# Performance work log

Measured on AMD Instinct MI355X. Metric: run time of the kernel, lower is better.

## Reference

```python
import jax, jax.numpy as jnp
import numpy as np

N_NODES = 100000
N_EDGES = 1600000
D_IN = 128
D_OUT = 128


def setup_inputs() -> dict:
    key = jax.random.key(0)
    k1, k2, k3 = jax.random.split(key, 3)
    x = jax.random.normal(k1, (N_NODES, D_IN), dtype=jnp.float32)
    edge_index = jax.random.randint(k2, (2, N_EDGES), 0, N_NODES, dtype=jnp.int32)
    W = jax.random.normal(k3, (D_IN, D_OUT), dtype=jnp.float32) / np.sqrt(D_IN)
    b = jnp.zeros((D_OUT,), dtype=jnp.float32)
    return {"x": x, "edge_index": edge_index, "W": W, "b": b}


def reference(x, edge_index, W, b):
    """GCNConv (add self-loops, symmetric norm) + ReLU.
    out = relu(D^-1/2 (A+I) D^-1/2 X W + b)
    """
    N = x.shape[0]
    src, dst = edge_index[0], edge_index[1]
    loop = jnp.arange(N, dtype=src.dtype)
    src = jnp.concatenate([src, loop])  # [E+N]
    dst = jnp.concatenate([dst, loop])  # [E+N]

    # degree of target nodes (includes self-loop, so deg >= 1)
    deg = jax.ops.segment_sum(jnp.ones(dst.shape, dtype=x.dtype), dst,
                              num_segments=N)
    deg_inv_sqrt = jax.lax.rsqrt(deg)
    norm = deg_inv_sqrt[src] * deg_inv_sqrt[dst]  # [E+N]

    h = x @ W  # [N, D_OUT] — transform before aggregation (PyG GCNConv)
    msg = h[src] * norm[:, None]  # gather + normalize
    out = jax.ops.segment_sum(msg, dst, num_segments=N)  # scatter-add
    return jax.nn.relu(out + b)
```

## Files before the change

kernel.cpp:

```cpp
#include <hip/hip_runtime.h>

#define N_NODES 100000
#define N_EDGES 1600000
#define D 128
#define SUBW 64
#define NSUB 1563
#define NC 98
#define CAPC 20480
#define CAP3 18432
#define CAPS 2048
#define CHUNK3 4096
#define BIND_BLOCKS ((N_EDGES + CHUNK3 - 1) / CHUNK3)
#define STAGE_MAX (CHUNK3 + NC * 16)
#define CCSTRIDE 16

typedef __attribute__((ext_vector_type(8))) short short8;
typedef __attribute__((ext_vector_type(4))) float float4v;

__device__ inline unsigned short f2bf(float f) {
    unsigned u = __float_as_uint(f);
    unsigned r = (u + 0x7fffu + ((u >> 16) & 1u)) >> 16;
    return (unsigned short)r;
}
__device__ inline float bflo(unsigned int p) { return __uint_as_float(p << 16); }
__device__ inline float bfhi(unsigned int p) { return __uint_as_float(p & 0xffff0000u); }

__global__ void probe_convert_kernel(const unsigned int* __restrict__ xw,
                                     const void* __restrict__ b,
                                     int* __restrict__ flag, float* __restrict__ bfv) {
    __shared__ int cnt;
    if (threadIdx.x == 0) cnt = 0;
    __syncthreads();
    unsigned low = xw[threadIdx.x] & 0xFFFFu;
    unsigned e = (low >> 7) & 0xFFu;
    atomicAdd(&cnt, (int)((e == 0u) || (e >= 107u && e <= 147u)));
    __syncthreads();
    int m = (cnt >= 192);
    if (threadIdx.x == 0) *flag = m;
    if (threadIdx.x < D)
        bfv[threadIdx.x] = m ? bflo(((const unsigned short*)b)[threadIdx.x])
                             : ((const float*)b)[threadIdx.x];
}

__global__ void __launch_bounds__(256) binD_kernel(
        const int* __restrict__ src, const int* __restrict__ dst,
        int* __restrict__ ccnt, unsigned* __restrict__ recg) {
    __shared__ __align__(16) unsigned stg[STAGE_MAX];
    __shared__ int cnt[NC], cpad[NC], ofs[NC], base[NC], place[NC];
    __shared__ int tot;

    int tid = threadIdx.x;
    int e0 = blockIdx.x * CHUNK3;
    int e1 = e0 + CHUNK3 < N_EDGES ? e0 + CHUNK3 : N_EDGES;
    if (tid < NC) cnt[tid] = 0;
    __syncthreads();

    unsigned recs[16];
    int bks[16];
    #pragma unroll
    for (int k = 0; k < 4; ++k) {
        int i = e0 + tid * 4 + k * 1024;
        if (i + 3 < e1) {
            int4 d4 = *(const int4*)&dst[i];
            int4 s4 = *(const int4*)&src[i];
            recs[k * 4 + 0] = (unsigned)s4.x | ((unsigned)(d4.x & 1023) << 17); bks[k * 4 + 0] = d4.x >> 10;
            recs[k * 4 + 1] = (unsigned)s4.y | ((unsigned)(d4.y & 1023) << 17); bks[k * 4 + 1] = d4.y >> 10;
            recs[k * 4 + 2] = (unsigned)s4.z | ((unsigned)(d4.z & 1023) << 17); bks[k * 4 + 2] = d4.z >> 10;
            recs[k * 4 + 3] = (unsigned)s4.w | ((unsigned)(d4.w & 1023) << 17); bks[k * 4 + 3] = d4.w >> 10;
        } else {
            bks[k * 4 + 0] = -1; bks[k * 4 + 1] = -1; bks[k * 4 + 2] = -1; bks[k * 4 + 3] = -1;
            recs[k * 4 + 0] = 0; recs[k * 4 + 1] = 0; recs[k * 4 + 2] = 0; recs[k * 4 + 3] = 0;
        }
    }
    #pragma unroll
    for (int k = 0; k < 16; ++k)
        if (bks[k] >= 0) atomicAdd(&cnt[bks[k]], 1);
    __syncthreads();

    if (tid < NC) {
        int c = cnt[tid];
        int p = (c + 15) & ~15;
        cpad[tid] = p;
        base[tid] = p ? atomicAdd(&ccnt[tid * CCSTRIDE], p) : 0;
    }
    __syncthreads();
    if (tid == 0) {
        int s = 0;
        for (int k = 0; k < NC; ++k) { ofs[k] = s; place[k] = s; s += cpad[k]; }
        tot = s;
    }
    __syncthreads();
    if (tid < NC) {
        int e = ofs[tid] + cpad[tid];
        for (int j = ofs[tid] + cnt[tid]; j < e; ++j) stg[j] = 0xFFFFFFFFu;
    }
    __syncthreads();

    #pragma unroll
    for (int k = 0; k < 16; ++k)
        if (bks[k] >= 0) {
            int p = atomicAdd(&place[bks[k]], 1);
            stg[p] = recs[k];
        }
    __syncthreads();

    int tot_ = tot;
    for (int j = tid * 4; j < tot_; j += 1024) {
        int lo = 0, hi = NC - 1;
        while (lo < hi) { int mid = (lo + hi + 1) >> 1; if (ofs[mid] <= j) lo = mid; else hi = mid - 1; }
        int gi = base[lo] + (j - ofs[lo]);
        if (gi < CAPC)
            *(uint4*)&recg[(size_t)lo * CAPC + gi] = *(const uint4*)&stg[j];
    }
}

__global__ void __launch_bounds__(256) sortdeg_kernel(
        unsigned* __restrict__ recg, const int* __restrict__ ccnt,
        int* __restrict__ deg, int* __restrict__ nodeofs) {
    __shared__ int hist[1024];
    __shared__ int ofs[1024];
    __shared__ int place[1024];
    __shared__ int wsum[4];
    __shared__ __align__(16) unsigned s_srt[CAP3];

    int b = blockIdx.x, tid = threadIdx.x;
    for (int t = tid; t < 1024; t += 256) hist[t] = 0;
    __syncthreads();
    int count = ccnt[b * CCSTRIDE]; if (count > CAPC) count = CAPC;
    const unsigned* r = recg + (size_t)b * CAPC;
    for (int i = tid * 4; i + 3 < count; i += 1024) {
        uint4 w4 = *(const uint4*)&r[i];
        if (w4.x != 0xFFFFFFFFu) atomicAdd(&hist[w4.x >> 17], 1);
        if (w4.y != 0xFFFFFFFFu) atomicAdd(&hist[w4.y >> 17], 1);
        if (w4.z != 0xFFFFFFFFu) atomicAdd(&hist[w4.z >> 17], 1);
        if (w4.w != 0xFFFFFFFFu) atomicAdd(&hist[w4.w >> 17], 1);
    }
    __syncthreads();

    int h0 = hist[tid * 4], h1 = hist[tid * 4 + 1];
    int h2 = hist[tid * 4 + 2], h3 = hist[tid * 4 + 3];
    int tot_t = h0 + h1 + h2 + h3;
    int lane = tid & 63, wave = tid >> 6;
    int v = tot_t;
    #pragma unroll
    for (int dsh = 1; dsh < 64; dsh <<= 1) {
        int u = __shfl_up(v, dsh);
        if (lane >= dsh) v += u;
    }
    if (lane == 63) wsum[wave] = v;
    __syncthreads();
    int wbase = 0;
    #pragma unroll
    for (int k = 0; k < 4; ++k) if (k < wave) wbase += wsum[k];
    int e0v = wbase + v - tot_t;
    ofs[tid * 4]     = e0v;           place[tid * 4]     = e0v;
    ofs[tid * 4 + 1] = e0v + h0;      place[tid * 4 + 1] = e0v + h0;
    ofs[tid * 4 + 2] = e0v + h0 + h1; place[tid * 4 + 2] = e0v + h0 + h1;
    ofs[tid * 4 + 3] = e0v + h0 + h1 + h2;
    place[tid * 4 + 3] = e0v + h0 + h1 + h2;
    int n4 = b * 1024 + tid * 4;
    *(int4*)&deg[n4]     = make_int4(h0, h1, h2, h3);
    *(int4*)&nodeofs[n4] = make_int4(e0v, e0v + h0, e0v + h0 + h1, e0v + h0 + h1 + h2);
    __syncthreads();

    for (int i = tid * 4; i + 3 < count; i += 1024) {
        uint4 w4 = *(const uint4*)&r[i];
        if (w4.x != 0xFFFFFFFFu) { int p = atomicAdd(&place[w4.x >> 17], 1); if (p < CAP3) s_srt[p] = w4.x & 0x1FFFFu; }
        if (w4.y != 0xFFFFFFFFu) { int p = atomicAdd(&place[w4.y >> 17], 1); if (p < CAP3) s_srt[p] = w4.y & 0x1FFFFu; }
        if (w4.z != 0xFFFFFFFFu) { int p = atomicAdd(&place[w4.z >> 17], 1); if (p < CAP3) s_srt[p] = w4.z & 0x1FFFFu; }
        if (w4.w != 0xFFFFFFFFu) { int p = atomicAdd(&place[w4.w >> 17], 1); if (p < CAP3) s_srt[p] = w4.w & 0x1FFFFu; }
    }
    __syncthreads();

    int total = ofs[1023] + hist[1023];
    int totR = (total + 15) & ~15; if (totR > CAP3) totR = CAP3;
    unsigned* w = recg + (size_t)b * CAPC;
    for (int j = tid * 4; j < totR; j += 1024)
        *(uint4*)&w[j] = *(const uint4*)&s_srt[j];
}

__global__ void gemm_kernel(const void* __restrict__ xv, const void* __restrict__ Wv,
                            const int* __restrict__ flag, const int* __restrict__ deg,
                            unsigned short* __restrict__ h) {
    __shared__ unsigned short Wt[D * 136];
    int tid = threadIdx.x;
    int m = *flag;
    for (int idx = tid; idx < D * D; idx += 256) {
        int k = idx >> 7, c = idx & 127;
        Wt[c * 136 + k] = m ? ((const unsigned short*)Wv)[idx]
                            : f2bf(((const float*)Wv)[idx]);
    }
    __syncthreads();

    int wave = tid >> 6, lane = tid & 63;
    int row0 = (blockIdx.x * 4 + wave) * 16;
    if (row0 >= N_NODES) return;
    int r = lane & 15, quad = lane >> 4;

    short8 a[4];
    if (m) {
        const unsigned short* xr = (const unsigned short*)xv + (size_t)(row0 + r) * D + quad * 8;
        #pragma unroll
        for (int t = 0; t < 4; ++t) a[t] = *(const short8*)(xr + t * 32);
    } else {
        const float* xr = (const float*)xv + (size_t)(row0 + r) * D + quad * 8;
        #pragma unroll
        for (int t = 0; t < 4; ++t)
            for (int j = 0; j < 8; ++j) a[t][j] = (short)f2bf(xr[t * 32 + j]);
    }

    float sc[4];
    #pragma unroll
    for (int reg = 0; reg < 4; ++reg)
        sc[reg] = rsqrtf((float)(deg[row0 + quad * 4 + reg] + 1));

    #pragma unroll
    for (int ct = 0; ct < 8; ++ct) {
        int col0 = ct * 16;
        float4v c = {0.f, 0.f, 0.f, 0.f};
        #pragma unroll
        for (int t = 0; t < 4; ++t) {
            short8 bfr = *(const short8*)&Wt[(col0 + r) * 136 + t * 32 + quad * 8];
            c = __builtin_amdgcn_mfma_f32_16x16x32_bf16(a[t], bfr, c, 0, 0, 0);
        }
        #pragma unroll
        for (int reg = 0; reg < 4; ++reg) {
            int orow = row0 + quad * 4 + reg;
            h[(size_t)orow * D + col0 + r] = f2bf(c[reg] * sc[reg]);
        }
    }
}

__global__ void __launch_bounds__(256) agg4_kernel(
        const unsigned* __restrict__ srt2, const int* __restrict__ nodeofs,
        const int* __restrict__ deg,
        const float* __restrict__ bfv, const int* __restrict__ flag,
        const unsigned short* __restrict__ h, void* __restrict__ out) {
    __shared__ unsigned srt[CAPS];
    __shared__ int l_ofs[SUBW];
    __shared__ int l_deg[SUBW];
    __shared__ float lbias[D];

    int sub = blockIdx.x, tid = threadIdx.x;
    int n0 = sub * SUBW;
    int B = sub >> 4, loc0 = (sub & 15) * SUBW;
    if (tid < SUBW) {
        l_ofs[tid] = nodeofs[B * 1024 + loc0 + tid];
        int n = n0 + tid;
        l_deg[tid] = (n < N_NODES) ? deg[n] : 0;
    }
    if (tid < D) lbias[tid] = bfv[tid];
    __syncthreads();

    int base0 = l_ofs[0];
    int span = (l_ofs[SUBW - 1] + l_deg[SUBW - 1]) - base0;
    if (span > CAPS) span = CAPS;
    if (span > CAP3 - base0) span = CAP3 - base0;
    const unsigned* sb = srt2 + (size_t)B * CAPC + base0;
    for (int i = tid; i < span; i += 256) srt[i] = sb[i];
    __syncthreads();

    const uint4* h4 = (const uint4*)h;
    int wave = tid >> 6, lane = tid & 63;
    int q = lane >> 4, c16 = lane & 15;
    int m = *flag;

    for (int t = 0; t < 16; ++t) {
        int nl = wave * 16 + t;
        int n = n0 + nl;
        if (n >= N_NODES) break;
        int o = l_ofs[nl] - base0;
        int cnt = l_deg[nl];
        int e_end = o + cnt; if (e_end > span) e_end = span;

        uint4 sp = make_uint4(0u, 0u, 0u, 0u);
        if (q == 0) sp = h4[(size_t)n * 16 + c16];

        float acc[8] = {0.f, 0.f, 0.f, 0.f, 0.f, 0.f, 0.f, 0.f};
        int j = o + q;
        for (; j + 4 < e_end; j += 8) {
            unsigned s0 = srt[j];
            unsigned s1 = srt[j + 4];
            uint4 p0 = h4[(size_t)s0 * 16 + c16];
            uint4 p1 = h4[(size_t)s1 * 16 + c16];
            acc[0] += bflo(p0.x); acc[1] += bfhi(p0.x);
            acc[2] += bflo(p0.y); acc[3] += bfhi(p0.y);
            acc[4] += bflo(p0.z); acc[5] += bfhi(p0.z);
            acc[6] += bflo(p0.w); acc[7] += bfhi(p0.w);
            acc[0] += bflo(p1.x); acc[1] += bfhi(p1.x);
            acc[2] += bflo(p1.y); acc[3] += bfhi(p1.y);
            acc[4] += bflo(p1.z); acc[5] += bfhi(p1.z);
            acc[6] += bflo(p1.w); acc[7] += bfhi(p1.w);
        }
        if (j < e_end) {
            unsigned s0 = srt[j];
            uint4 p0 = h4[(size_t)s0 * 16 + c16];
            acc[0] += bflo(p0.x); acc[1] += bfhi(p0.x);
            acc[2] += bflo(p0.y); acc[3] += bfhi(p0.y);
            acc[4] += bflo(p0.z); acc[5] += bfhi(p0.z);
            acc[6] += bflo(p0.w); acc[7] += bfhi(p0.w);
        }
        #pragma unroll
        for (int i = 0; i < 8; ++i) {
            acc[i] += __shfl_xor(acc[i], 16);
            acc[i] += __shfl_xor(acc[i], 32);
        }

        if (q == 0) {
            float dn = rsqrtf((float)(cnt + 1));
            float v[8];
            v[0] = fmaxf(dn * (acc[0] + bflo(sp.x)) + lbias[c16 * 8 + 0], 0.f);
            v[1] = fmaxf(dn * (acc[1] + bfhi(sp.x)) + lbias[c16 * 8 + 1], 0.f);
            v[2] = fmaxf(dn * (acc[2] + bflo(sp.y)) + lbias[c16 * 8 + 2], 0.f);
            v[3] = fmaxf(dn * (acc[3] + bfhi(sp.y)) + lbias[c16 * 8 + 3], 0.f);
            v[4] = fmaxf(dn * (acc[4] + bflo(sp.z)) + lbias[c16 * 8 + 4], 0.f);
            v[5] = fmaxf(dn * (acc[5] + bfhi(sp.z)) + lbias[c16 * 8 + 5], 0.f);
            v[6] = fmaxf(dn * (acc[6] + bflo(sp.w)) + lbias[c16 * 8 + 6], 0.f);
            v[7] = fmaxf(dn * (acc[7] + bfhi(sp.w)) + lbias[c16 * 8 + 7], 0.f);
            if (m) {
                uint4 pk;
                pk.x = ((unsigned)f2bf(v[1]) << 16) | f2bf(v[0]);
                pk.y = ((unsigned)f2bf(v[3]) << 16) | f2bf(v[2]);
                pk.z = ((unsigned)f2bf(v[5]) << 16) | f2bf(v[4]);
                pk.w = ((unsigned)f2bf(v[7]) << 16) | f2bf(v[6]);
                ((uint4*)out)[(size_t)n * 16 + c16] = pk;
            } else {
                float4 f0 = make_float4(v[0], v[1], v[2], v[3]);
                float4 f1 = make_float4(v[4], v[5], v[6], v[7]);
                float4* of = (float4*)((float*)out + (size_t)n * D + c16 * 8);
                of[0] = f0; of[1] = f1;
            }
        }
    }
}

extern "C" void kernel_launch(void* const* d_in, const int* in_sizes, int n_in,
                              void* d_out, int out_size, void* d_ws, size_t ws_size,
                              hipStream_t stream) {
    const void* x = nullptr; const int* ei = nullptr;
    const void* W = nullptr; const void* b = nullptr;
    for (int i = 0; i < n_in; ++i) {
        if      (in_sizes[i] == N_NODES * D) x  = d_in[i];
        else if (in_sizes[i] == 2 * N_EDGES) ei = (const int*)d_in[i];
        else if (in_sizes[i] == D * D)       W  = d_in[i];
        else if (in_sizes[i] == D)           b  = d_in[i];
    }
    if (!x || !ei || !W || !b) {
        x = d_in[0]; ei = (const int*)d_in[1]; W = d_in[2]; b = d_in[3];
    }
    const int* src = ei;
    const int* dst = ei + N_EDGES;

    char* ws = (char*)d_ws;
    int*      flag    = (int*)ws;
    int*      ccnt    = (int*)(ws + 16);
    float*    bfv     = (float*)(ccnt + NC * CCSTRIDE);
    int*      deg     = (int*)(bfv + D);
    int*      nodeofs = deg + NC * 1024;
    unsigned* recg    = (unsigned*)(nodeofs + NC * 1024);
    unsigned short* h = (unsigned short*)(recg + (size_t)NC * CAPC);

    hipMemsetAsync(ccnt, 0, sizeof(int) * NC * CCSTRIDE, stream);

    probe_convert_kernel<<<1, 256, 0, stream>>>((const unsigned int*)x, b, flag, bfv);

    binD_kernel<<<BIND_BLOCKS, 256, 0, stream>>>(src, dst, ccnt, recg);

    sortdeg_kernel<<<NC, 256, 0, stream>>>(recg, ccnt, deg, nodeofs);

    gemm_kernel<<<NSUB, 256, 0, stream>>>(x, W, flag, deg, h);

    agg4_kernel<<<NSUB, 256, 0, stream>>>(recg, nodeofs, deg, bfv, flag, h, d_out);
}
```

Measured before the change: 276.4 us.

## Fuse edge binning with GEMM and move source-degree scaling into aggregation

```diff
diff --git a/kernel.cpp b/kernel.cpp
--- a/kernel.cpp
+++ b/kernel.cpp
@@ -3,14 +3,15 @@
 #define N_NODES 100000
 #define N_EDGES 1600000
 #define D 128
-#define SUBW 64
-#define NSUB 1563
+#define SUBW 32
+#define NSUB2 3125
 #define NC 98
 #define CAPC 20480
 #define CAP3 18432
-#define CAPS 2048
+#define CAPS2 1024
 #define CHUNK3 4096
 #define BIND_BLOCKS ((N_EDGES + CHUNK3 - 1) / CHUNK3)
+#define GEMM_BLOCKS ((N_NODES + 63) / 64)
 #define STAGE_MAX (CHUNK3 + NC * 16)
 #define CCSTRIDE 16
 
@@ -27,7 +28,8 @@
 
 __global__ void probe_convert_kernel(const unsigned int* __restrict__ xw,
                                      const void* __restrict__ b,
-                                     int* __restrict__ flag, float* __restrict__ bfv) {
+                                     int* __restrict__ flag, float* __restrict__ bfv,
+                                     int* __restrict__ ccnt) {
     __shared__ int cnt;
     if (threadIdx.x == 0) cnt = 0;
     __syncthreads();
@@ -40,83 +42,142 @@
     if (threadIdx.x < D)
         bfv[threadIdx.x] = m ? bflo(((const unsigned short*)b)[threadIdx.x])
                              : ((const float*)b)[threadIdx.x];
-}
-
-__global__ void __launch_bounds__(256) binD_kernel(
+    for (int i = threadIdx.x; i < NC * CCSTRIDE; i += 256) ccnt[i] = 0;
+}
+
+__global__ void __launch_bounds__(256) fused_bingemm_kernel(
         const int* __restrict__ src, const int* __restrict__ dst,
-        int* __restrict__ ccnt, unsigned* __restrict__ recg) {
-    __shared__ __align__(16) unsigned stg[STAGE_MAX];
-    __shared__ int cnt[NC], cpad[NC], ofs[NC], base[NC], place[NC];
-    __shared__ int tot;
+        int* __restrict__ ccnt, unsigned* __restrict__ recg,
+        const void* __restrict__ xv, const void* __restrict__ Wv,
+        const int* __restrict__ flag, unsigned short* __restrict__ h) {
+    __shared__ union {
+        struct {
+            unsigned stg[STAGE_MAX];
+            int cnt[NC], cpad[NC], ofs[NC], base[NC], place[NC];
+            int tot;
+        } b;
+        unsigned short Wt[D * 136];
+    } u;
 
     int tid = threadIdx.x;
-    int e0 = blockIdx.x * CHUNK3;
-    int e1 = e0 + CHUNK3 < N_EDGES ? e0 + CHUNK3 : N_EDGES;
-    if (tid < NC) cnt[tid] = 0;
-    __syncthreads();
-
-    unsigned recs[16];
-    int bks[16];
-    #pragma unroll
-    for (int k = 0; k < 4; ++k) {
-        int i = e0 + tid * 4 + k * 1024;
-        if (i + 3 < e1) {
-            int4 d4 = *(const int4*)&dst[i];
-            int4 s4 = *(const int4*)&src[i];
-            recs[k * 4 + 0] = (unsigned)s4.x | ((unsigned)(d4.x & 1023) << 17); bks[k * 4 + 0] = d4.x >> 10;
-            recs[k * 4 + 1] = (unsigned)s4.y | ((unsigned)(d4.y & 1023) << 17); bks[k * 4 + 1] = d4.y >> 10;
-            recs[k * 4 + 2] = (unsigned)s4.z | ((unsigned)(d4.z & 1023) << 17); bks[k * 4 + 2] = d4.z >> 10;
-            recs[k * 4 + 3] = (unsigned)s4.w | ((unsigned)(d4.w & 1023) << 17); bks[k * 4 + 3] = d4.w >> 10;
+
+    if (blockIdx.x < BIND_BLOCKS) {
+        int e0 = blockIdx.x * CHUNK3;
+        int e1 = e0 + CHUNK3 < N_EDGES ? e0 + CHUNK3 : N_EDGES;
+        if (tid < NC) u.b.cnt[tid] = 0;
+        __syncthreads();
+
+        unsigned recs[16];
+        int bks[16];
+        #pragma unroll
+        for (int k = 0; k < 4; ++k) {
+            int i = e0 + tid * 4 + k * 1024;
+            if (i + 3 < e1) {
+                int4 d4 = *(const int4*)&dst[i];
+                int4 s4 = *(const int4*)&src[i];
+                recs[k * 4 + 0] = (unsigned)s4.x | ((unsigned)(d4.x & 1023) << 17); bks[k * 4 + 0] = d4.x >> 10;
+                recs[k * 4 + 1] = (unsigned)s4.y | ((unsigned)(d4.y & 1023) << 17); bks[k * 4 + 1] = d4.y >> 10;
+                recs[k * 4 + 2] = (unsigned)s4.z | ((unsigned)(d4.z & 1023) << 17); bks[k * 4 + 2] = d4.z >> 10;
+                recs[k * 4 + 3] = (unsigned)s4.w | ((unsigned)(d4.w & 1023) << 17); bks[k * 4 + 3] = d4.w >> 10;
+            } else {
+                bks[k * 4 + 0] = -1; bks[k * 4 + 1] = -1; bks[k * 4 + 2] = -1; bks[k * 4 + 3] = -1;
+                recs[k * 4 + 0] = 0; recs[k * 4 + 1] = 0; recs[k * 4 + 2] = 0; recs[k * 4 + 3] = 0;
+            }
+        }
+        #pragma unroll
+        for (int k = 0; k < 16; ++k)
+            if (bks[k] >= 0) atomicAdd(&u.b.cnt[bks[k]], 1);
+        __syncthreads();
+
+        if (tid < NC) {
+            int c = u.b.cnt[tid];
+            int p = (c + 15) & ~15;
+            u.b.cpad[tid] = p;
+            u.b.base[tid] = p ? atomicAdd(&ccnt[tid * CCSTRIDE], p) : 0;
+        }
+        __syncthreads();
+        if (tid == 0) {
+            int s = 0;
+            for (int k = 0; k < NC; ++k) { u.b.ofs[k] = s; u.b.place[k] = s; s += u.b.cpad[k]; }
+            u.b.tot = s;
+        }
+        __syncthreads();
+        if (tid < NC) {
+            int e = u.b.ofs[tid] + u.b.cpad[tid];
+            for (int j = u.b.ofs[tid] + u.b.cnt[tid]; j < e; ++j) u.b.stg[j] = 0xFFFFFFFFu;
+        }
+        __syncthreads();
+
+        #pragma unroll
+        for (int k = 0; k < 16; ++k)
+            if (bks[k] >= 0) {
+                int p = atomicAdd(&u.b.place[bks[k]], 1);
+                u.b.stg[p] = recs[k];
+            }
+        __syncthreads();
+
+        int tot_ = u.b.tot;
+        for (int j = tid * 4; j < tot_; j += 1024) {
+            int lo = 0, hi = NC - 1;
+            while (lo < hi) { int mid = (lo + hi + 1) >> 1; if (u.b.ofs[mid] <= j) lo = mid; else hi = mid - 1; }
+            int gi = u.b.base[lo] + (j - u.b.ofs[lo]);
+            if (gi < CAPC)
+                *(uint4*)&recg[(size_t)lo * CAPC + gi] = *(const uint4*)&u.b.stg[j];
+        }
+    } else {
+        int bid2 = blockIdx.x - BIND_BLOCKS;
+        int m = *flag;
+        for (int idx = tid; idx < D * D; idx += 256) {
+            int k = idx >> 7, c = idx & 127;
+            u.Wt[c * 136 + k] = m ? ((const unsigned short*)Wv)[idx]
+                                  : f2bf(((const float*)Wv)[idx]);
+        }
+        __syncthreads();
+
+        int wave = tid >> 6, lane = tid & 63;
+        int row0 = (bid2 * 4 + wave) * 16;
+        if (row0 >= N_NODES) return;
+        int r = lane & 15, quad = lane >> 4;
+
+        short8 a[4];
+        if (m) {
+            const unsigned short* xr = (const unsigned short*)xv + (size_t)(row0 + r) * D + quad * 8;
+            #pragma unroll
+            for (int t = 0; t < 4; ++t) a[t] = *(const short8*)(xr + t * 32);
         } else {
-            bks[k * 4 + 0] = -1; bks[k * 4 + 1] = -1; bks[k * 4 + 2] = -1; bks[k * 4 + 3] = -1;
-            recs[k * 4 + 0] = 0; recs[k * 4 + 1] = 0; recs[k * 4 + 2] = 0; recs[k * 4 + 3] = 0;
-        }
-    }
-    #pragma unroll
-    for (int k = 0; k < 16; ++k)
-        if (bks[k] >= 0) atomicAdd(&cnt[bks[k]], 1);
-    __syncthreads();
-
-    if (tid < NC) {
-        int c = cnt[tid];
-        int p = (c + 15) & ~15;
-        cpad[tid] = p;
-        base[tid] = p ? atomicAdd(&ccnt[tid * CCSTRIDE], p) : 0;
-    }
-    __syncthreads();
-    if (tid == 0) {
-        int s = 0;
-        for (int k = 0; k < NC; ++k) { ofs[k] = s; place[k] = s; s += cpad[k]; }
-        tot = s;
-    }
-    __syncthreads();
-    if (tid < NC) {
-        int e = ofs[tid] + cpad[tid];
-        for (int j = ofs[tid] + cnt[tid]; j < e; ++j) stg[j] = 0xFFFFFFFFu;
-    }
-    __syncthreads();
-
-    #pragma unroll
-    for (int k = 0; k < 16; ++k)
-        if (bks[k] >= 0) {
-            int p = atomicAdd(&place[bks[k]], 1);
-            stg[p] = recs[k];
-        }
-    __syncthreads();
-
-    int tot_ = tot;
-    for (int j = tid * 4; j < tot_; j += 1024) {
-        int lo = 0, hi = NC - 1;
-        while (lo < hi) { int mid = (lo + hi + 1) >> 1; if (ofs[mid] <= j) lo = mid; else hi = mid - 1; }
-        int gi = base[lo] + (j - ofs[lo]);
-        if (gi < CAPC)
-            *(uint4*)&recg[(size_t)lo * CAPC + gi] = *(const uint4*)&stg[j];
+            const float* xr = (const float*)xv + (size_t)(row0 + r) * D + quad * 8;
+            #pragma unroll
+            for (int t = 0; t < 4; ++t) {
+                float4 f0 = *(const float4*)(xr + t * 32);
+                float4 f1 = *(const float4*)(xr + t * 32 + 4);
+                a[t][0] = (short)f2bf(f0.x); a[t][1] = (short)f2bf(f0.y);
+                a[t][2] = (short)f2bf(f0.z); a[t][3] = (short)f2bf(f0.w);
+                a[t][4] = (short)f2bf(f1.x); a[t][5] = (short)f2bf(f1.y);
+                a[t][6] = (short)f2bf(f1.z); a[t][7] = (short)f2bf(f1.w);
+            }
+        }
+
+        #pragma unroll
+        for (int ct = 0; ct < 8; ++ct) {
+            int col0 = ct * 16;
+            float4v c = {0.f, 0.f, 0.f, 0.f};
+            #pragma unroll
+            for (int t = 0; t < 4; ++t) {
+                short8 bfr = *(const short8*)&u.Wt[(col0 + r) * 136 + t * 32 + quad * 8];
+                c = __builtin_amdgcn_mfma_f32_16x16x32_bf16(a[t], bfr, c, 0, 0, 0);
+            }
+            #pragma unroll
+            for (int reg = 0; reg < 4; ++reg) {
+                int orow = row0 + quad * 4 + reg;
+                h[(size_t)orow * D + col0 + r] = f2bf(c[reg]);
+            }
+        }
     }
 }
 
 __global__ void __launch_bounds__(256) sortdeg_kernel(
         unsigned* __restrict__ recg, const int* __restrict__ ccnt,
-        int* __restrict__ deg, int* __restrict__ nodeofs) {
+        int* __restrict__ deg, int* __restrict__ nodeofs, float* __restrict__ dis) {
     __shared__ int hist[1024];
     __shared__ int ofs[1024];
     __shared__ int place[1024];
@@ -144,8 +205,8 @@
     int v = tot_t;
     #pragma unroll
     for (int dsh = 1; dsh < 64; dsh <<= 1) {
-        int u = __shfl_up(v, dsh);
-        if (lane >= dsh) v += u;
+        int uu = __shfl_up(v, dsh);
+        if (lane >= dsh) v += uu;
     }
     if (lane == 63) wsum[wave] = v;
     __syncthreads();
@@ -161,6 +222,8 @@
     int n4 = b * 1024 + tid * 4;
     *(int4*)&deg[n4]     = make_int4(h0, h1, h2, h3);
     *(int4*)&nodeofs[n4] = make_int4(e0v, e0v + h0, e0v + h0 + h1, e0v + h0 + h1 + h2);
+    *(float4*)&dis[n4]   = make_float4(rsqrtf((float)(h0 + 1)), rsqrtf((float)(h1 + 1)),
+                                       rsqrtf((float)(h2 + 1)), rsqrtf((float)(h3 + 1)));
     __syncthreads();
 
     for (int i = tid * 4; i + 3 < count; i += 1024) {
@@ -179,82 +242,29 @@
         *(uint4*)&w[j] = *(const uint4*)&s_srt[j];
 }
 
-__global__ void gemm_kernel(const void* __restrict__ xv, const void* __restrict__ Wv,
-                            const int* __restrict__ flag, const int* __restrict__ deg,
-                            unsigned short* __restrict__ h) {
-    __shared__ unsigned short Wt[D * 136];
-    int tid = threadIdx.x;
-    int m = *flag;
-    for (int idx = tid; idx < D * D; idx += 256) {
-        int k = idx >> 7, c = idx & 127;
-        Wt[c * 136 + k] = m ? ((const unsigned short*)Wv)[idx]
-                            : f2bf(((const float*)Wv)[idx]);
-    }
-    __syncthreads();
-
-    int wave = tid >> 6, lane = tid & 63;
-    int row0 = (blockIdx.x * 4 + wave) * 16;
-    if (row0 >= N_NODES) return;
-    int r = lane & 15, quad = lane >> 4;
-
-    short8 a[4];
-    if (m) {
-        const unsigned short* xr = (const unsigned short*)xv + (size_t)(row0 + r) * D + quad * 8;
-        #pragma unroll
-        for (int t = 0; t < 4; ++t) a[t] = *(const short8*)(xr + t * 32);
-    } else {
-        const float* xr = (const float*)xv + (size_t)(row0 + r) * D + quad * 8;
-        #pragma unroll
-        for (int t = 0; t < 4; ++t)
-            for (int j = 0; j < 8; ++j) a[t][j] = (short)f2bf(xr[t * 32 + j]);
-    }
-
-    float sc[4];
-    #pragma unroll
-    for (int reg = 0; reg < 4; ++reg)
-        sc[reg] = rsqrtf((float)(deg[row0 + quad * 4 + reg] + 1));
-
-    #pragma unroll
-    for (int ct = 0; ct < 8; ++ct) {
-        int col0 = ct * 16;
-        float4v c = {0.f, 0.f, 0.f, 0.f};
-        #pragma unroll
-        for (int t = 0; t < 4; ++t) {
-            short8 bfr = *(const short8*)&Wt[(col0 + r) * 136 + t * 32 + quad * 8];
-            c = __builtin_amdgcn_mfma_f32_16x16x32_bf16(a[t], bfr, c, 0, 0, 0);
-        }
-        #pragma unroll
-        for (int reg = 0; reg < 4; ++reg) {
-            int orow = row0 + quad * 4 + reg;
-            h[(size_t)orow * D + col0 + r] = f2bf(c[reg] * sc[reg]);
-        }
-    }
-}
-
-__global__ void __launch_bounds__(256) agg4_kernel(
+__global__ void __launch_bounds__(256) agg5_kernel(
         const unsigned* __restrict__ srt2, const int* __restrict__ nodeofs,
-        const int* __restrict__ deg,
+        const int* __restrict__ deg, const float* __restrict__ dis,
         const float* __restrict__ bfv, const int* __restrict__ flag,
         const unsigned short* __restrict__ h, void* __restrict__ out) {
-    __shared__ unsigned srt[CAPS];
+    __shared__ unsigned srt[CAPS2];
     __shared__ int l_ofs[SUBW];
     __shared__ int l_deg[SUBW];
     __shared__ float lbias[D];
 
     int sub = blockIdx.x, tid = threadIdx.x;
     int n0 = sub * SUBW;
-    int B = sub >> 4, loc0 = (sub & 15) * SUBW;
+    int B = n0 >> 10, loc0 = n0 & 1023;
     if (tid < SUBW) {
         l_ofs[tid] = nodeofs[B * 1024 + loc0 + tid];
-        int n = n0 + tid;
-        l_deg[tid] = (n < N_NODES) ? deg[n] : 0;
+        l_deg[tid] = deg[n0 + tid];
     }
     if (tid < D) lbias[tid] = bfv[tid];
     __syncthreads();
 
     int base0 = l_ofs[0];
     int span = (l_ofs[SUBW - 1] + l_deg[SUBW - 1]) - base0;
-    if (span > CAPS) span = CAPS;
+    if (span > CAPS2) span = CAPS2;
     if (span > CAP3 - base0) span = CAP3 - base0;
     const unsigned* sb = srt2 + (size_t)B * CAPC + base0;
     for (int i = tid; i < span; i += 256) srt[i] = sb[i];
@@ -265,10 +275,9 @@
     int q = lane >> 4, c16 = lane & 15;
     int m = *flag;
 
-    for (int t = 0; t < 16; ++t) {
-        int nl = wave * 16 + t;
+    for (int t = 0; t < 8; ++t) {
+        int nl = wave * 8 + t;
         int n = n0 + nl;
-        if (n >= N_NODES) break;
         int o = l_ofs[nl] - base0;
         int cnt = l_deg[nl];
         int e_end = o + cnt; if (e_end > span) e_end = span;
@@ -283,22 +292,24 @@
             unsigned s1 = srt[j + 4];
             uint4 p0 = h4[(size_t)s0 * 16 + c16];
             uint4 p1 = h4[(size_t)s1 * 16 + c16];
-            acc[0] += bflo(p0.x); acc[1] += bfhi(p0.x);
-            acc[2] += bflo(p0.y); acc[3] += bfhi(p0.y);
-            acc[4] += bflo(p0.z); acc[5] += bfhi(p0.z);
-            acc[6] += bflo(p0.w); acc[7] += bfhi(p0.w);
-            acc[0] += bflo(p1.x); acc[1] += bfhi(p1.x);
-            acc[2] += bflo(p1.y); acc[3] += bfhi(p1.y);
-            acc[4] += bflo(p1.z); acc[5] += bfhi(p1.z);
-            acc[6] += bflo(p1.w); acc[7] += bfhi(p1.w);
+            float w0 = dis[s0], w1 = dis[s1];
+            acc[0] += w0 * bflo(p0.x); acc[1] += w0 * bfhi(p0.x);
+            acc[2] += w0 * bflo(p0.y); acc[3] += w0 * bfhi(p0.y);
+            acc[4] += w0 * bflo(p0.z); acc[5] += w0 * bfhi(p0.z);
+            acc[6] += w0 * bflo(p0.w); acc[7] += w0 * bfhi(p0.w);
+            acc[0] += w1 * bflo(p1.x); acc[1] += w1 * bfhi(p1.x);
+            acc[2] += w1 * bflo(p1.y); acc[3] += w1 * bfhi(p1.y);
+            acc[4] += w1 * bflo(p1.z); acc[5] += w1 * bfhi(p1.z);
+            acc[6] += w1 * bflo(p1.w); acc[7] += w1 * bfhi(p1.w);
         }
         if (j < e_end) {
             unsigned s0 = srt[j];
             uint4 p0 = h4[(size_t)s0 * 16 + c16];
-            acc[0] += bflo(p0.x); acc[1] += bfhi(p0.x);
-            acc[2] += bflo(p0.y); acc[3] += bfhi(p0.y);
-            acc[4] += bflo(p0.z); acc[5] += bfhi(p0.z);
-            acc[6] += bflo(p0.w); acc[7] += bfhi(p0.w);
+            float w0 = dis[s0];
+            acc[0] += w0 * bflo(p0.x); acc[1] += w0 * bfhi(p0.x);
+            acc[2] += w0 * bflo(p0.y); acc[3] += w0 * bfhi(p0.y);
+            acc[4] += w0 * bflo(p0.z); acc[5] += w0 * bfhi(p0.z);
+            acc[6] += w0 * bflo(p0.w); acc[7] += w0 * bfhi(p0.w);
         }
         #pragma unroll
         for (int i = 0; i < 8; ++i) {
@@ -309,14 +320,14 @@
         if (q == 0) {
             float dn = rsqrtf((float)(cnt + 1));
             float v[8];
-            v[0] = fmaxf(dn * (acc[0] + bflo(sp.x)) + lbias[c16 * 8 + 0], 0.f);
-            v[1] = fmaxf(dn * (acc[1] + bfhi(sp.x)) + lbias[c16 * 8 + 1], 0.f);
-            v[2] = fmaxf(dn * (acc[2] + bflo(sp.y)) + lbias[c16 * 8 + 2], 0.f);
-            v[3] = fmaxf(dn * (acc[3] + bfhi(sp.y)) + lbias[c16 * 8 + 3], 0.f);
-            v[4] = fmaxf(dn * (acc[4] + bflo(sp.z)) + lbias[c16 * 8 + 4], 0.f);
-            v[5] = fmaxf(dn * (acc[5] + bfhi(sp.z)) + lbias[c16 * 8 + 5], 0.f);
-            v[6] = fmaxf(dn * (acc[6] + bflo(sp.w)) + lbias[c16 * 8 + 6], 0.f);
-            v[7] = fmaxf(dn * (acc[7] + bfhi(sp.w)) + lbias[c16 * 8 + 7], 0.f);
+            v[0] = fmaxf(dn * (acc[0] + dn * bflo(sp.x)) + lbias[c16 * 8 + 0], 0.f);
+            v[1] = fmaxf(dn * (acc[1] + dn * bfhi(sp.x)) + lbias[c16 * 8 + 1], 0.f);
+            v[2] = fmaxf(dn * (acc[2] + dn * bflo(sp.y)) + lbias[c16 * 8 + 2], 0.f);
+            v[3] = fmaxf(dn * (acc[3] + dn * bfhi(sp.y)) + lbias[c16 * 8 + 3], 0.f);
+            v[4] = fmaxf(dn * (acc[4] + dn * bflo(sp.z)) + lbias[c16 * 8 + 4], 0.f);
+            v[5] = fmaxf(dn * (acc[5] + dn * bfhi(sp.z)) + lbias[c16 * 8 + 5], 0.f);
+            v[6] = fmaxf(dn * (acc[6] + dn * bflo(sp.w)) + lbias[c16 * 8 + 6], 0.f);
+            v[7] = fmaxf(dn * (acc[7] + dn * bfhi(sp.w)) + lbias[c16 * 8 + 7], 0.f);
             if (m) {
                 uint4 pk;
                 pk.x = ((unsigned)f2bf(v[1]) << 16) | f2bf(v[0]);
@@ -357,18 +368,16 @@
     float*    bfv     = (float*)(ccnt + NC * CCSTRIDE);
     int*      deg     = (int*)(bfv + D);
     int*      nodeofs = deg + NC * 1024;
-    unsigned* recg    = (unsigned*)(nodeofs + NC * 1024);
+    float*    dis     = (float*)(nodeofs + NC * 1024);
+    unsigned* recg    = (unsigned*)(dis + NC * 1024);
     unsigned short* h = (unsigned short*)(recg + (size_t)NC * CAPC);
 
-    hipMemsetAsync(ccnt, 0, sizeof(int) * NC * CCSTRIDE, stream);
-
-    probe_convert_kernel<<<1, 256, 0, stream>>>((const unsigned int*)x, b, flag, bfv);
-
-    binD_kernel<<<BIND_BLOCKS, 256, 0, stream>>>(src, dst, ccnt, recg);
-
-    sortdeg_kernel<<<NC, 256, 0, stream>>>(recg, ccnt, deg, nodeofs);
-
-    gemm_kernel<<<NSUB, 256, 0, stream>>>(x, W, flag, deg, h);
-
-    agg4_kernel<<<NSUB, 256, 0, stream>>>(recg, nodeofs, deg, bfv, flag, h, d_out);
-}
+    probe_convert_kernel<<<1, 256, 0, stream>>>((const unsigned int*)x, b, flag, bfv, ccnt);
+
+    fused_bingemm_kernel<<<BIND_BLOCKS + GEMM_BLOCKS, 256, 0, stream>>>(
+        src, dst, ccnt, recg, x, W, flag, h);
+
+    sortdeg_kernel<<<NC, 256, 0, stream>>>(recg, ccnt, deg, nodeofs, dis);
+
+    agg5_kernel<<<NSUB2, 256, 0, stream>>>(recg, nodeofs, deg, dis, bfv, flag, h, d_out);
+}
```

After: 256.9 us. 1.08x faster.
